# Kernel optimization log

Hardware: AMD Instinct MI355X
Metric: run time of the kernel (lower is better)

Reference implementation:

```python
import jax, jax.numpy as jnp
import numpy as np
import math

N = 16
ZIGZAG = np.array([135, 150, 165, 180, 195, 210, 225, 240, 241, 226, 211, 196, 181, 166, 151, 136, 121, 106, 91, 76, 61, 46, 31, 47, 62, 77, 92, 107, 122, 137, 152, 167, 182, 197, 212, 227, 242, 243, 228, 213, 198, 183, 168, 153, 138, 123, 108, 93, 78, 63, 79, 94, 109, 124, 139, 154, 169, 184, 199, 214, 229, 244, 245, 230, 215, 200, 185, 170, 155, 140, 125, 110, 95, 111, 126, 141, 156, 171, 186, 201, 216, 231, 246, 247, 232, 217, 202, 187, 172, 157, 142, 127, 143, 158, 173, 188, 203, 218, 233, 248, 249, 234, 219, 204, 189, 174, 159, 175, 190, 205, 220, 235, 250, 251, 236, 221, 206, 191, 207, 222, 237, 252, 253, 238, 223, 239, 254, 255], dtype=np.int32)

# DCT basis (harmonics) and normalization matrix, matching the torch helpers
_i = np.arange(N, dtype=np.float32)
HARM = np.cos((2.0 * _i[:, None] + 1.0) * (_i[None, :] * math.pi / (2.0 * N))).astype(np.float32)
_n = np.ones((N, 1), dtype=np.float32); _n[0, 0] = 1.0 / math.sqrt(2.0)
NMAT = (_n @ _n.T).astype(np.float32)
SCALE = 1.0 / math.sqrt(2.0 * N)


def setup_inputs() -> dict:
    key = jax.random.key(0)
    x = jax.random.normal(key, (8, 3, 1024, 1024), dtype=jnp.float32)
    return {"x": x}


def reference(x):
    b, c, h, w = x.shape
    # blockify: [b, c, n_blocks, 16, 16], blocks in row-major spatial order
    blocks = x.reshape(b, c, h // N, N, w // N, N).transpose(0, 1, 2, 4, 3, 5).reshape(b, c, -1, N, N)
    harm = jnp.asarray(HARM)
    nmat = jnp.asarray(NMAT)
    # block DCT: scale * n * (H^T @ block @ H)
    coeff = SCALE * nmat * (jnp.matmul(jnp.matmul(harm.T, blocks), harm))
    # zigzag upper-band gather: [b, c, n_blocks, 128]
    flat = coeff.reshape(b, c, -1, N * N)[..., jnp.asarray(ZIGZAG)]
    # adaptive threshold: zero out coefficients below per-block mean
    mean = jnp.mean(flat, axis=3, keepdims=True)
    sel = jnp.where(flat < mean, jnp.float32(0), flat)
    a = jnp.abs(sel) + 1e-12
    # L2 normalize along coefficient dim (torch F.normalize, eps=1e-12)
    norm = jnp.sqrt(jnp.sum(a * a, axis=3, keepdims=True))
    probs = a / jnp.maximum(norm, 1e-12)
    log_prob = jnp.log2(probs)
    entropy = jnp.mean(-jnp.sum(probs * log_prob, axis=3))
    return entropy
```

## Files before the change

### kernel.cpp

```cpp
#include <hip/hip_runtime.h>
#include <stdint.h>


typedef float f32x4 __attribute__((ext_vector_type(4)));
typedef short bf16x8 __attribute__((ext_vector_type(8)));

constexpr double kPi = 3.14159265358979323846;

constexpr double ccos(double x) {
    while (x > kPi) x -= 2.0 * kPi;
    while (x < -kPi) x += 2.0 * kPi;
    double x2 = x * x;
    double term = 1.0, sum = 1.0;
    for (int k = 1; k <= 24; ++k) {
        term *= -x2 / (double)((2 * k - 1) * (2 * k));
        sum += term;
    }
    return sum;
}

constexpr float fharm(int i, int f) {
    float colf = (float)((double)f * kPi) / 32.0f;
    float arg = (2.0f * (float)i + 1.0f) * colf;
    return (float)ccos((double)arg);
}

constexpr uint16_t f2bf(float f) {
    unsigned u = __builtin_bit_cast(unsigned, f);
    return (uint16_t)((u + 0x7fffu + ((u >> 16) & 1u)) >> 16);
}

struct FragTables {
    alignas(16) uint32_t blo[64][4];
    alignas(16) uint32_t bhi[64][4];
    alignas(16) uint32_t a2[64][4];
    constexpr FragTables() : blo{}, bhi{}, a2{} {
        for (int l = 0; l < 64; ++l) {
            const int n = l & 15;
            const int q = l >> 4;
            uint16_t slo[8] = {}, shi[8] = {}, sa[8] = {};
            for (int s = 0; s < 8; ++s) {
                const int k = 8 * q + s;
                if (k < 16) {
                    float g = fharm(k, n) *
                              ((n == 0) ? 0.70710678118654752440f : 1.0f);
                    slo[s] = f2bf(g);
                    sa[s] = f2bf(g * 0.17677669529663688110f);
                } else {
                    float g = fharm(k - 16, n) *
                              ((n == 0) ? 0.70710678118654752440f : 1.0f);
                    shi[s] = f2bf(g);
                }
            }
            for (int d = 0; d < 4; ++d) {
                blo[l][d] = (uint32_t)slo[2 * d] | ((uint32_t)slo[2 * d + 1] << 16);
                bhi[l][d] = (uint32_t)shi[2 * d] | ((uint32_t)shi[2 * d + 1] << 16);
                a2[l][d] = (uint32_t)sa[2 * d] | ((uint32_t)sa[2 * d + 1] << 16);
            }
        }
    }
};
__constant__ FragTables kF{};

#define NWG 6144
#define NPART (NWG * 4)

#define WAVE_LDS_FENCE() asm volatile("s_waitcnt lgkmcnt(0)" ::: "memory")

__device__ __forceinline__ uint32_t bfr(float f) {
    uint32_t u = __float_as_uint(f);
    return (u + 0x7fffu + ((u >> 16) & 1u)) >> 16;
}
__device__ __forceinline__ uint32_t pk2(float a, float b) {
    return bfr(a) | (bfr(b) << 16);
}

__global__ __launch_bounds__(256, 4) void dct_entropy_kernel(
    const float* __restrict__ x, float* __restrict__ partials) {
    __shared__ float smem[4 * 1344];

    const int t = threadIdx.x;
    const int wave = t >> 6;
    const int lane = t & 63;
    const int l15 = lane & 15;
    const int q = lane >> 4;
    float* R = smem + wave * 1344;
    uint32_t* Rw = (uint32_t*)R;

    const int g = blockIdx.x;
    const int bc = g >> 8;
    const int br = (g >> 2) & 63;
    const int cg = g & 3;
    const float* gbase =
        x + ((size_t)bc << 20) + ((size_t)br << 14) + (cg << 8) + (wave << 6);

    const float* rp = gbase + (size_t)l15 * 1024 + 8 * q;
    float4 lo0 = *(const float4*)(rp);
    float4 hi0 = *(const float4*)(rp + 4);
    float4 lo1 = *(const float4*)(rp + 32);
    float4 hi1 = *(const float4*)(rp + 36);

    const bf16x8 fBlo = __builtin_bit_cast(bf16x8, *(const uint4*)kF.blo[lane]);
    const bf16x8 fBhi = __builtin_bit_cast(bf16x8, *(const uint4*)kF.bhi[lane]);
    const bf16x8 fA2 = __builtin_bit_cast(bf16x8, *(const uint4*)kF.a2[lane]);

    uint4 ua0 = {pk2(lo0.x, lo0.y), pk2(lo0.z, lo0.w),
                 pk2(hi0.x, hi0.y), pk2(hi0.z, hi0.w)};
    uint4 ua1 = {pk2(lo1.x, lo1.y), pk2(lo1.z, lo1.w),
                 pk2(hi1.x, hi1.y), pk2(hi1.z, hi1.w)};
    const bf16x8 fA0 = __builtin_bit_cast(bf16x8, ua0);
    const bf16x8 fA1 = __builtin_bit_cast(bf16x8, ua1);

    const f32x4 z = {0.0f, 0.0f, 0.0f, 0.0f};
    f32x4 W0 = __builtin_amdgcn_mfma_f32_16x16x32_bf16(fA0, fBlo, z, 0, 0, 0);
    f32x4 W1 = __builtin_amdgcn_mfma_f32_16x16x32_bf16(fA0, fBhi, z, 0, 0, 0);
    f32x4 W2 = __builtin_amdgcn_mfma_f32_16x16x32_bf16(fA1, fBlo, z, 0, 0, 0);
    f32x4 W3 = __builtin_amdgcn_mfma_f32_16x16x32_bf16(fA1, fBhi, z, 0, 0, 0);

    {
        const int wi = 12 * l15 + 2 * q;
        *(uint2*)(&Rw[wi]) = make_uint2(pk2(W0.x, W0.y), pk2(W0.z, W0.w));
        *(uint2*)(&Rw[192 + wi]) = make_uint2(pk2(W1.x, W1.y), pk2(W1.z, W1.w));
        *(uint2*)(&Rw[384 + wi]) = make_uint2(pk2(W2.x, W2.y), pk2(W2.z, W2.w));
        *(uint2*)(&Rw[576 + wi]) = make_uint2(pk2(W3.x, W3.y), pk2(W3.z, W3.w));
    }
    WAVE_LDS_FENCE();

    bf16x8 fW[4];
    {
        const int ri = 12 * l15 + 4 * (q & 1);
#pragma unroll
        for (int b = 0; b < 4; ++b)
            fW[b] = __builtin_bit_cast(bf16x8, *(const uint4*)(&Rw[192 * b + ri]));
    }
    WAVE_LDS_FENCE();

    {
#pragma unroll
        for (int b = 0; b < 4; ++b) {
            f32x4 C = __builtin_amdgcn_mfma_f32_16x16x32_bf16(fA2, fW[b], z, 0, 0, 0);
            *(f32x4*)(&R[324 * b + 20 * l15 + 4 * q]) = C;
        }
    }
    WAVE_LDS_FENCE();

    {
        const float* C = &R[324 * q + 20 * l15];
        float c[16];
#pragma unroll
        for (int k = 0; k < 4; ++k) {
            float4 f = *(const float4*)(C + 4 * k);
            c[4 * k + 0] = f.x;
            c[4 * k + 1] = f.y;
            c[4 * k + 2] = f.z;
            c[4 * k + 3] = f.w;
        }
        const int v = l15;
        const int u_min = (v > 7) ? (16 - v) : (15 - v);

        float s = 0.0f;
#pragma unroll
        for (int u = 0; u < 16; ++u) s += (u >= u_min) ? c[u] : 0.0f;
#pragma unroll
        for (int m = 1; m <= 8; m <<= 1) s += __shfl_xor(s, m);
        const float mean = s * (1.0f / 128.0f);

        float a[16];
        float sq = 0.0f;
#pragma unroll
        for (int u = 0; u < 16; ++u) {
            float au = (c[u] < mean) ? 1e-12f : (fabsf(c[u]) + 1e-12f);
            a[u] = (u >= u_min) ? au : 0.0f;
            sq = fmaf(a[u], a[u], sq);
        }
#pragma unroll
        for (int m = 1; m <= 8; m <<= 1) sq += __shfl_xor(sq, m);
        const float inv = 1.0f / fmaxf(sqrtf(sq), 1e-12f);

        float e = 0.0f;
#pragma unroll
        for (int u = 0; u < 16; ++u) {
            float p = a[u] * inv;
            float term = p * __log2f(p);
            e += (u >= u_min) ? term : 0.0f;
        }
#pragma unroll
        for (int m = 1; m <= 32; m <<= 1) e += __shfl_xor(e, m);
        if (lane == 0) partials[(g << 2) + wave] = e;
    }
}

__global__ __launch_bounds__(1024) void reduce_partials(
    const float* __restrict__ partials, float* __restrict__ out) {
    __shared__ float s[16];
    float v = 0.0f;
    const float4* p4 = (const float4*)partials;
    for (int i = threadIdx.x; i < NPART / 4; i += 1024) {
        float4 f = p4[i];
        v += (f.x + f.y) + (f.z + f.w);
    }
#pragma unroll
    for (int m = 1; m <= 32; m <<= 1) v += __shfl_xor(v, m);
    if ((threadIdx.x & 63) == 0) s[threadIdx.x >> 6] = v;
    __syncthreads();
    if (threadIdx.x < 16) {
        float tot = s[threadIdx.x];
#pragma unroll
        for (int m = 1; m <= 8; m <<= 1) tot += __shfl_xor(tot, m);
        if (threadIdx.x == 0) out[0] = tot * (-1.0f / 98304.0f);
    }
}

extern "C" void kernel_launch(void* const* d_in, const int* in_sizes, int n_in,
                              void* d_out, int out_size, void* d_ws,
                              size_t ws_size, hipStream_t stream) {
    const float* x = (const float*)d_in[0];
    float* out = (float*)d_out;
    float* ws = (float*)d_ws;
    dct_entropy_kernel<<<NWG, 256, 0, stream>>>(x, ws);
    reduce_partials<<<1, 1024, 0, stream>>>(ws, out);
}
```

Before: 144.3 us.

## Process four strips per wave with register prefetch of next strip

Reduces the grid from 6144 to 1536 workgroups. Each wave now loops over four 16x64 strips, loading the next strip's global data into registers while the current strip's MFMA and entropy work runs. This is meant to hide global load latency and spread the constant-table loads and launch overhead over more work. The final reduction kernel shrinks to 256 threads with a fixed unrolled loop. The tradeoff is fewer resident waves to hide latency and somewhat higher register pressure.

```diff
diff --git a/kernel.cpp b/kernel.cpp
--- a/kernel.cpp
+++ b/kernel.cpp
@@ -62,7 +62,7 @@
 };
 __constant__ FragTables kF{};
 
-#define NWG 6144
+#define NWG 1536
 #define NPART (NWG * 4)
 
 #define WAVE_LDS_FENCE() asm volatile("s_waitcnt lgkmcnt(0)" ::: "memory")
@@ -88,126 +88,155 @@
     uint32_t* Rw = (uint32_t*)R;
 
     const int g = blockIdx.x;
-    const int bc = g >> 8;
-    const int br = (g >> 2) & 63;
-    const int cg = g & 3;
-    const float* gbase =
-        x + ((size_t)bc << 20) + ((size_t)br << 14) + (cg << 8) + (wave << 6);
-
-    const float* rp = gbase + (size_t)l15 * 1024 + 8 * q;
+
+    const int s0 = (g << 4) + wave;
+
+    const size_t lane_off = (size_t)l15 * 1024 + 8 * q;
+
+    auto strip_ptr = [&](int it) -> const float* {
+        const int s = s0 + (it << 2);
+        const int bc = s >> 10;
+        const int br = (s >> 4) & 63;
+        const int cs = s & 15;
+        return x + ((size_t)bc << 20) + ((size_t)br << 14) + (cs << 6) +
+               lane_off;
+    };
+
+    const bf16x8 fBlo = __builtin_bit_cast(bf16x8, *(const uint4*)kF.blo[lane]);
+    const bf16x8 fBhi = __builtin_bit_cast(bf16x8, *(const uint4*)kF.bhi[lane]);
+    const bf16x8 fA2 = __builtin_bit_cast(bf16x8, *(const uint4*)kF.a2[lane]);
+    const f32x4 z = {0.0f, 0.0f, 0.0f, 0.0f};
+
+    const float* rp = strip_ptr(0);
     float4 lo0 = *(const float4*)(rp);
     float4 hi0 = *(const float4*)(rp + 4);
     float4 lo1 = *(const float4*)(rp + 32);
     float4 hi1 = *(const float4*)(rp + 36);
 
-    const bf16x8 fBlo = __builtin_bit_cast(bf16x8, *(const uint4*)kF.blo[lane]);
-    const bf16x8 fBhi = __builtin_bit_cast(bf16x8, *(const uint4*)kF.bhi[lane]);
-    const bf16x8 fA2 = __builtin_bit_cast(bf16x8, *(const uint4*)kF.a2[lane]);
-
-    uint4 ua0 = {pk2(lo0.x, lo0.y), pk2(lo0.z, lo0.w),
-                 pk2(hi0.x, hi0.y), pk2(hi0.z, hi0.w)};
-    uint4 ua1 = {pk2(lo1.x, lo1.y), pk2(lo1.z, lo1.w),
-                 pk2(hi1.x, hi1.y), pk2(hi1.z, hi1.w)};
-    const bf16x8 fA0 = __builtin_bit_cast(bf16x8, ua0);
-    const bf16x8 fA1 = __builtin_bit_cast(bf16x8, ua1);
-
-    const f32x4 z = {0.0f, 0.0f, 0.0f, 0.0f};
-    f32x4 W0 = __builtin_amdgcn_mfma_f32_16x16x32_bf16(fA0, fBlo, z, 0, 0, 0);
-    f32x4 W1 = __builtin_amdgcn_mfma_f32_16x16x32_bf16(fA0, fBhi, z, 0, 0, 0);
-    f32x4 W2 = __builtin_amdgcn_mfma_f32_16x16x32_bf16(fA1, fBlo, z, 0, 0, 0);
-    f32x4 W3 = __builtin_amdgcn_mfma_f32_16x16x32_bf16(fA1, fBhi, z, 0, 0, 0);
-
-    {
-        const int wi = 12 * l15 + 2 * q;
-        *(uint2*)(&Rw[wi]) = make_uint2(pk2(W0.x, W0.y), pk2(W0.z, W0.w));
-        *(uint2*)(&Rw[192 + wi]) = make_uint2(pk2(W1.x, W1.y), pk2(W1.z, W1.w));
-        *(uint2*)(&Rw[384 + wi]) = make_uint2(pk2(W2.x, W2.y), pk2(W2.z, W2.w));
-        *(uint2*)(&Rw[576 + wi]) = make_uint2(pk2(W3.x, W3.y), pk2(W3.z, W3.w));
-    }
-    WAVE_LDS_FENCE();
-
-    bf16x8 fW[4];
-    {
-        const int ri = 12 * l15 + 4 * (q & 1);
-#pragma unroll
-        for (int b = 0; b < 4; ++b)
-            fW[b] = __builtin_bit_cast(bf16x8, *(const uint4*)(&Rw[192 * b + ri]));
-    }
-    WAVE_LDS_FENCE();
-
-    {
-#pragma unroll
-        for (int b = 0; b < 4; ++b) {
-            f32x4 C = __builtin_amdgcn_mfma_f32_16x16x32_bf16(fA2, fW[b], z, 0, 0, 0);
-            *(f32x4*)(&R[324 * b + 20 * l15 + 4 * q]) = C;
-        }
-    }
-    WAVE_LDS_FENCE();
-
-    {
-        const float* C = &R[324 * q + 20 * l15];
-        float c[16];
-#pragma unroll
-        for (int k = 0; k < 4; ++k) {
-            float4 f = *(const float4*)(C + 4 * k);
-            c[4 * k + 0] = f.x;
-            c[4 * k + 1] = f.y;
-            c[4 * k + 2] = f.z;
-            c[4 * k + 3] = f.w;
-        }
-        const int v = l15;
-        const int u_min = (v > 7) ? (16 - v) : (15 - v);
-
-        float s = 0.0f;
-#pragma unroll
-        for (int u = 0; u < 16; ++u) s += (u >= u_min) ? c[u] : 0.0f;
-#pragma unroll
-        for (int m = 1; m <= 8; m <<= 1) s += __shfl_xor(s, m);
-        const float mean = s * (1.0f / 128.0f);
-
-        float a[16];
-        float sq = 0.0f;
-#pragma unroll
-        for (int u = 0; u < 16; ++u) {
-            float au = (c[u] < mean) ? 1e-12f : (fabsf(c[u]) + 1e-12f);
-            a[u] = (u >= u_min) ? au : 0.0f;
-            sq = fmaf(a[u], a[u], sq);
-        }
-#pragma unroll
-        for (int m = 1; m <= 8; m <<= 1) sq += __shfl_xor(sq, m);
-        const float inv = 1.0f / fmaxf(sqrtf(sq), 1e-12f);
-
-        float e = 0.0f;
-#pragma unroll
-        for (int u = 0; u < 16; ++u) {
-            float p = a[u] * inv;
-            float term = p * __log2f(p);
-            e += (u >= u_min) ? term : 0.0f;
-        }
-#pragma unroll
-        for (int m = 1; m <= 32; m <<= 1) e += __shfl_xor(e, m);
-        if (lane == 0) partials[(g << 2) + wave] = e;
-    }
-}
-
-__global__ __launch_bounds__(1024) void reduce_partials(
+    float etot = 0.0f;
+
+#pragma unroll
+    for (int it = 0; it < 4; ++it) {
+        uint4 ua0 = {pk2(lo0.x, lo0.y), pk2(lo0.z, lo0.w),
+                     pk2(hi0.x, hi0.y), pk2(hi0.z, hi0.w)};
+        uint4 ua1 = {pk2(lo1.x, lo1.y), pk2(lo1.z, lo1.w),
+                     pk2(hi1.x, hi1.y), pk2(hi1.z, hi1.w)};
+        const bf16x8 fA0 = __builtin_bit_cast(bf16x8, ua0);
+        const bf16x8 fA1 = __builtin_bit_cast(bf16x8, ua1);
+
+        if (it < 3) {
+            const float* np = strip_ptr(it + 1);
+            lo0 = *(const float4*)(np);
+            hi0 = *(const float4*)(np + 4);
+            lo1 = *(const float4*)(np + 32);
+            hi1 = *(const float4*)(np + 36);
+        }
+
+        f32x4 W0 = __builtin_amdgcn_mfma_f32_16x16x32_bf16(fA0, fBlo, z, 0, 0, 0);
+        f32x4 W1 = __builtin_amdgcn_mfma_f32_16x16x32_bf16(fA0, fBhi, z, 0, 0, 0);
+        f32x4 W2 = __builtin_amdgcn_mfma_f32_16x16x32_bf16(fA1, fBlo, z, 0, 0, 0);
+        f32x4 W3 = __builtin_amdgcn_mfma_f32_16x16x32_bf16(fA1, fBhi, z, 0, 0, 0);
+
+        WAVE_LDS_FENCE();
+
+        {
+            const int wi = 12 * l15 + 2 * q;
+            *(uint2*)(&Rw[wi]) = make_uint2(pk2(W0.x, W0.y), pk2(W0.z, W0.w));
+            *(uint2*)(&Rw[192 + wi]) =
+                make_uint2(pk2(W1.x, W1.y), pk2(W1.z, W1.w));
+            *(uint2*)(&Rw[384 + wi]) =
+                make_uint2(pk2(W2.x, W2.y), pk2(W2.z, W2.w));
+            *(uint2*)(&Rw[576 + wi]) =
+                make_uint2(pk2(W3.x, W3.y), pk2(W3.z, W3.w));
+        }
+        WAVE_LDS_FENCE();
+
+        bf16x8 fW[4];
+        {
+            const int ri = 12 * l15 + 4 * (q & 1);
+#pragma unroll
+            for (int b = 0; b < 4; ++b)
+                fW[b] = __builtin_bit_cast(bf16x8,
+                                           *(const uint4*)(&Rw[192 * b + ri]));
+        }
+        WAVE_LDS_FENCE();
+
+        {
+#pragma unroll
+            for (int b = 0; b < 4; ++b) {
+                f32x4 C = __builtin_amdgcn_mfma_f32_16x16x32_bf16(fA2, fW[b],
+                                                                  z, 0, 0, 0);
+                *(f32x4*)(&R[324 * b + 20 * l15 + 4 * q]) = C;
+            }
+        }
+        WAVE_LDS_FENCE();
+
+        {
+            const float* C = &R[324 * q + 20 * l15];
+            float c[16];
+#pragma unroll
+            for (int k = 0; k < 4; ++k) {
+                float4 f = *(const float4*)(C + 4 * k);
+                c[4 * k + 0] = f.x;
+                c[4 * k + 1] = f.y;
+                c[4 * k + 2] = f.z;
+                c[4 * k + 3] = f.w;
+            }
+            const int v = l15;
+            const int u_min = (v > 7) ? (16 - v) : (15 - v);
+
+            float s = 0.0f;
+#pragma unroll
+            for (int u = 0; u < 16; ++u) s += (u >= u_min) ? c[u] : 0.0f;
+#pragma unroll
+            for (int m = 1; m <= 8; m <<= 1) s += __shfl_xor(s, m);
+            const float mean = s * (1.0f / 128.0f);
+
+            float a[16];
+            float sq = 0.0f;
+#pragma unroll
+            for (int u = 0; u < 16; ++u) {
+                float au = (c[u] < mean) ? 1e-12f : (fabsf(c[u]) + 1e-12f);
+                a[u] = (u >= u_min) ? au : 0.0f;
+                sq = fmaf(a[u], a[u], sq);
+            }
+#pragma unroll
+            for (int m = 1; m <= 8; m <<= 1) sq += __shfl_xor(sq, m);
+            const float inv = 1.0f / fmaxf(sqrtf(sq), 1e-12f);
+
+            float e = 0.0f;
+#pragma unroll
+            for (int u = 0; u < 16; ++u) {
+                float p = a[u] * inv;
+                float term = p * __log2f(p);
+                e += (u >= u_min) ? term : 0.0f;
+            }
+#pragma unroll
+            for (int m = 1; m <= 32; m <<= 1) e += __shfl_xor(e, m);
+            etot += e;
+        }
+    }
+
+    if (lane == 0) partials[(g << 2) + wave] = etot;
+}
+
+__global__ __launch_bounds__(256) void reduce_partials(
     const float* __restrict__ partials, float* __restrict__ out) {
-    __shared__ float s[16];
+    __shared__ float s[4];
     float v = 0.0f;
     const float4* p4 = (const float4*)partials;
-    for (int i = threadIdx.x; i < NPART / 4; i += 1024) {
-        float4 f = p4[i];
+#pragma unroll
+    for (int k = 0; k < NPART / 4 / 256; ++k) {
+        float4 f = p4[threadIdx.x + 256 * k];
         v += (f.x + f.y) + (f.z + f.w);
     }
 #pragma unroll
     for (int m = 1; m <= 32; m <<= 1) v += __shfl_xor(v, m);
     if ((threadIdx.x & 63) == 0) s[threadIdx.x >> 6] = v;
     __syncthreads();
-    if (threadIdx.x < 16) {
-        float tot = s[threadIdx.x];
-#pragma unroll
-        for (int m = 1; m <= 8; m <<= 1) tot += __shfl_xor(tot, m);
-        if (threadIdx.x == 0) out[0] = tot * (-1.0f / 98304.0f);
+    if (threadIdx.x == 0) {
+        float tot = (s[0] + s[1]) + (s[2] + s[3]);
+        out[0] = tot * (-1.0f / 98304.0f);
     }
 }
 
@@ -218,5 +247,5 @@
     float* out = (float*)d_out;
     float* ws = (float*)d_ws;
     dct_entropy_kernel<<<NWG, 256, 0, stream>>>(x, ws);
-    reduce_partials<<<1, 1024, 0, stream>>>(ws, out);
-}
+    reduce_partials<<<1, 256, 0, stream>>>(ws, out);
+}
```

Result: slower. 150.2 us (+4.1%).
